# Kernel optimization log

Hardware: AMD Instinct MI355X
Metric: run time of the kernel (lower is better)

## Reference

```python
import jax, jax.numpy as jnp
import numpy as np
from jax import lax

NUM_VARS = 16384
NUM_CHECKS = 8192
BATCH = 32
MAX_ITER = 15
H_DENSITY = 0.001  # ~8 ones per column, LDPC-like Tanner graph


def setup_inputs() -> dict:
    key = jax.random.key(0)
    k_h, k_s, k_l = jax.random.split(key, 3)
    # Sparse binary parity-check matrix represented densely (same math).
    parity_matrix = (jax.random.uniform(k_h, (NUM_CHECKS, NUM_VARS)) < H_DENSITY).astype(jnp.float32)
    syndrome = jax.random.randint(k_s, (BATCH, NUM_CHECKS), 0, 2).astype(jnp.float32)
    channel_llrs = jax.random.normal(k_l, (BATCH, NUM_VARS), dtype=jnp.float32)
    w_vc = jnp.ones((1,), dtype=jnp.float32)
    w_cv = jnp.ones((1,), dtype=jnp.float32)
    damping = jnp.float32(0.5)
    return {
        "syndrome": syndrome,
        "parity_matrix": parity_matrix,
        "channel_llrs": channel_llrs,
        "w_vc": w_vc,
        "w_cv": w_cv,
        "damping": damping,
    }


def reference(syndrome, parity_matrix, channel_llrs, w_vc, w_cv, damping):
    # syndrome: (B, C); parity_matrix H: (C, V); channel_llrs: (B, V)
    s_sign = 1.0 - 2.0 * syndrome  # (B, C)

    def body(v_beliefs, _):
        # v -> c: sparse.mm(H, v^T)^T == v @ H^T  -> (B, C)
        v_to_c = w_vc * (v_beliefs @ parity_matrix.T)
        c_msg = s_sign * jnp.tanh(v_to_c * 0.5)  # (B, C)
        # c -> v: sparse.mm(H^T, c^T)^T == c @ H  -> (B, V)
        c_to_v = w_cv * (c_msg @ parity_matrix)
        v_new = damping * v_beliefs + (1.0 - damping) * (channel_llrs + c_to_v)
        return v_new, None

    v_beliefs, _ = lax.scan(body, channel_llrs, None, length=MAX_ITER)
    return jax.nn.sigmoid(-v_beliefs)  # (B, V) bit-flip probabilities
```

## Files before the change

### kernel.cpp

```cpp
#include <hip/hip_runtime.h>


#define C_NUM 8192
#define V_NUM 16384
#define B_NUM 32
#define ROW_SLOTS 40
#define COL_SLOTS 24

#define NBLK 256
#define NTHR 1024
#define NTH (NBLK * NTHR)

typedef unsigned short u16;
typedef unsigned int u32;
typedef unsigned long long u64;

__device__ __forceinline__ float agent_ldf(const float* p) {
    return __hip_atomic_load(p, __ATOMIC_RELAXED, __HIP_MEMORY_SCOPE_AGENT);
}
__device__ __forceinline__ void agent_stf(float* p, float v) {
    __hip_atomic_store(p, v, __ATOMIC_RELAXED, __HIP_MEMORY_SCOPE_AGENT);
}
__device__ __forceinline__ u32 agent_ld32(const u32* p) {
    return __hip_atomic_load(p, __ATOMIC_RELAXED, __HIP_MEMORY_SCOPE_AGENT);
}
__device__ __forceinline__ void agent_st32(u32* p, u32 v) {
    __hip_atomic_store(p, v, __ATOMIC_RELAXED, __HIP_MEMORY_SCOPE_AGENT);
}
__device__ __forceinline__ int agent_ldi(const int* p) {
    return __hip_atomic_load(p, __ATOMIC_RELAXED, __HIP_MEMORY_SCOPE_AGENT);
}
__device__ __forceinline__ void agent_st16(u16* p, u16 v) {
    __hip_atomic_store(p, v, __ATOMIC_RELAXED, __HIP_MEMORY_SCOPE_AGENT);
}

__device__ __forceinline__ void grid_barrier(u32* flags, u32 ep) {
    __syncthreads();
    if (threadIdx.x < 64) {
        if (threadIdx.x == 0) {
            asm volatile("s_waitcnt vmcnt(0) lgkmcnt(0)" ::: "memory");
            agent_st32(&flags[blockIdx.x], ep);
        }
        const int base = threadIdx.x * 4;
        for (;;) {
            u32 f0 = agent_ld32(&flags[base + 0]);
            u32 f1 = agent_ld32(&flags[base + 1]);
            u32 f2 = agent_ld32(&flags[base + 2]);
            u32 f3 = agent_ld32(&flags[base + 3]);
            bool ok = (f0 >= ep) & (f1 >= ep) & (f2 >= ep) & (f3 >= ep);
            if (__ballot(ok) == ~0ull) break;
            __builtin_amdgcn_s_sleep(2);
        }
        asm volatile("" ::: "memory");
    }
    __syncthreads();
}

__device__ __forceinline__ float fast_tanh_half(float x) {
    float ax = fabsf(x);
    float e = __expf(-ax);
    return copysignf((1.0f - e) / (1.0f + e), x);
}

__global__ __launch_bounds__(NTHR, 4)
void bp_fused(const float* __restrict__ H,
              const float* __restrict__ synd,
              const float* __restrict__ llr,
              const float* __restrict__ w_vc_p,
              const float* __restrict__ w_cv_p,
              const float* __restrict__ damp_p,
              int* __restrict__ row_cnt, int* __restrict__ col_cnt,
              u16* __restrict__ row_tab, u16* __restrict__ col_tab,
              float* __restrict__ bel, float* __restrict__ cms,
              u32* __restrict__ flags,
              float* __restrict__ out) {
    const int tid = blockIdx.x * NTHR + threadIdx.x;
    u32 ep = 1;

    {
        u32* zp = (u32*)row_cnt;
        for (int t = tid; t < (C_NUM + V_NUM); t += NTH) agent_st32(&zp[t], 0u);
    }
    float llr_r[2], bel_r[2];
#pragma unroll
    for (int r = 0; r < 2; ++r) {
        int i = tid + r * NTH;
        int b = i & 31, v = i >> 5;
        float x = llr[b * V_NUM + v];
        llr_r[r] = x; bel_r[r] = x;
        agent_stf(&bel[i + 32], x);
    }
    float ss_r;
    {
        int b = tid & 31, c = tid >> 5;
        ss_r = 1.0f - 2.0f * synd[b * C_NUM + c];
    }
    grid_barrier(flags, ep++);

    {
        const int total4 = C_NUM * V_NUM / 4;
        const float4* Hv = (const float4*)H;
        for (int t = tid; t < total4; t += 2 * NTH) {
            float4 h0 = Hv[t];
            float4 h1 = Hv[t + NTH];
#pragma unroll
            for (int half = 0; half < 2; ++half) {
                float4 hv = half ? h1 : h0;
                int base = (half ? (t + NTH) : t) * 4;
                float vals[4] = {hv.x, hv.y, hv.z, hv.w};
#pragma unroll
                for (int k = 0; k < 4; ++k) {
                    if (vals[k] != 0.0f) {
                        int ee = base + k;
                        int c = ee >> 14;
                        int v = ee & (V_NUM - 1);
                        int rs = atomicAdd(&row_cnt[c], 1);
                        if (rs < ROW_SLOTS)
                            agent_st16(&row_tab[c * ROW_SLOTS + rs], (u16)(v + 1));
                        int cs = atomicAdd(&col_cnt[v], 1);
                        if (cs < COL_SLOTS)
                            agent_st16(&col_tab[v * COL_SLOTS + cs], (u16)(c + 1));
                    }
                }
            }
        }
    }
    grid_barrier(flags, ep++);

    if (tid < C_NUM) {
        int c = tid;
        int n = agent_ldi(&row_cnt[c]); n = n > ROW_SLOTS ? ROW_SLOTS : n;
        for (int k = n; k < ROW_SLOTS; ++k)
            agent_st16(&row_tab[c * ROW_SLOTS + k],
                       (u16)((((c * 97) + (k * 131)) & (V_NUM - 1)) + 1));
    } else if (tid < C_NUM + V_NUM) {
        int v = tid - C_NUM;
        int n = agent_ldi(&col_cnt[v]); n = n > COL_SLOTS ? COL_SLOTS : n;
        for (int k = n; k < COL_SLOTS; ++k)
            agent_st16(&col_tab[v * COL_SLOTS + k],
                       (u16)((((v * 89) + (k * 61)) & (C_NUM - 1)) + 1));
    }
    const float wvc = w_vc_p[0];
    const float wcv = w_cv_p[0];
    const float d   = damp_p[0];
    const int b  = tid & 31;
    const int c0 = tid >> 5;
    int n_row;
    {
        int n = agent_ldi(&row_cnt[c0]);
        n_row = n > ROW_SLOTS ? ROW_SLOTS : n;
    }
    int n_col[2];
#pragma unroll
    for (int r = 0; r < 2; ++r) {
        int n = agent_ldi(&col_cnt[(tid + r * NTH) >> 5]);
        n_col[r] = n > COL_SLOTS ? COL_SLOTS : n;
    }
    grid_barrier(flags, ep++);

    for (int it = 0; it < 15; ++it) {
        {
            const u64* rt = (const u64*)(row_tab + (size_t)c0 * ROW_SLOTS);
            float sum = 0.0f;
#pragma unroll
            for (int p = 0; p < ROW_SLOTS / 4; ++p) {
                u64 q = rt[p];
                float v0 = agent_ldf(&bel[(int)(q & 0xFFFFu) * 32 + b]);
                float v1 = agent_ldf(&bel[(int)((q >> 16) & 0xFFFFu) * 32 + b]);
                float v2 = agent_ldf(&bel[(int)((q >> 32) & 0xFFFFu) * 32 + b]);
                float v3 = agent_ldf(&bel[(int)(q >> 48) * 32 + b]);
                int j = p * 4;
                sum += (j     < n_row) ? v0 : 0.0f;
                sum += (j + 1 < n_row) ? v1 : 0.0f;
                sum += (j + 2 < n_row) ? v2 : 0.0f;
                sum += (j + 3 < n_row) ? v3 : 0.0f;
            }
            agent_stf(&cms[tid + 32], ss_r * fast_tanh_half(wvc * sum));
        }
        grid_barrier(flags, ep++);

        bool last = (it == 14);
#pragma unroll
        for (int r = 0; r < 2; ++r) {
            int i = tid + r * NTH;
            int v = i >> 5;
            const u64* ct = (const u64*)(col_tab + (size_t)v * COL_SLOTS);
            float sum = 0.0f;
#pragma unroll
            for (int p = 0; p < COL_SLOTS / 4; ++p) {
                u64 q = ct[p];
                float v0 = agent_ldf(&cms[(int)(q & 0xFFFFu) * 32 + b]);
                float v1 = agent_ldf(&cms[(int)((q >> 16) & 0xFFFFu) * 32 + b]);
                float v2 = agent_ldf(&cms[(int)((q >> 32) & 0xFFFFu) * 32 + b]);
                float v3 = agent_ldf(&cms[(int)(q >> 48) * 32 + b]);
                int j = p * 4;
                sum += (j     < n_col[r]) ? v0 : 0.0f;
                sum += (j + 1 < n_col[r]) ? v1 : 0.0f;
                sum += (j + 2 < n_col[r]) ? v2 : 0.0f;
                sum += (j + 3 < n_col[r]) ? v3 : 0.0f;
            }
            float nb = d * bel_r[r] + (1.0f - d) * (llr_r[r] + wcv * sum);
            bel_r[r] = nb;
            if (!last) agent_stf(&bel[i + 32], nb);
            else       out[b * V_NUM + v] = 1.0f / (1.0f + __expf(nb));
        }
        if (!last) grid_barrier(flags, ep++);
    }
}

extern "C" void kernel_launch(void* const* d_in, const int* in_sizes, int n_in,
                              void* d_out, int out_size, void* d_ws, size_t ws_size,
                              hipStream_t stream) {
    const float* synd = (const float*)d_in[0];
    const float* H    = (const float*)d_in[1];
    const float* llr  = (const float*)d_in[2];
    const float* w_vc = (const float*)d_in[3];
    const float* w_cv = (const float*)d_in[4];
    const float* damp = (const float*)d_in[5];
    float* out = (float*)d_out;

    char* ws = (char*)d_ws;
    size_t off = 0;
    int* row_cnt = (int*)(ws + off); off += (size_t)C_NUM * 4;
    int* col_cnt = (int*)(ws + off); off += (size_t)V_NUM * 4;
    u16* row_tab = (u16*)(ws + off); off += (size_t)C_NUM * ROW_SLOTS * 2;
    u16* col_tab = (u16*)(ws + off); off += (size_t)V_NUM * COL_SLOTS * 2;
    float* bel = (float*)(ws + off); off += (size_t)(V_NUM + 1) * 32 * 4;
    float* cms = (float*)(ws + off); off += (size_t)(C_NUM + 1) * 32 * 4;
    u32* flags = (u32*)(ws + off); off += (size_t)NBLK * 4;

    hipMemsetAsync(flags, 0, (size_t)NBLK * 4, stream);

    void* args[] = {
        (void*)&H, (void*)&synd, (void*)&llr,
        (void*)&w_vc, (void*)&w_cv, (void*)&damp,
        (void*)&row_cnt, (void*)&col_cnt, (void*)&row_tab, (void*)&col_tab,
        (void*)&bel, (void*)&cms, (void*)&flags, (void*)&out
    };
    hipLaunchCooperativeKernel((const void*)bp_fused,
                               dim3(NBLK), dim3(NTHR), args, 0, stream);
}
```

Measured before the change: 1.031 ms.

## Split batch into two half-chains with split-phase barriers to overlap iterations

Splits the 32-sample batch into two independent 16-sample chains, each with its own belief/check buffers and barrier flags. Grid barriers become split arrive/wait so one chain's phase runs while the other chain's barrier settles. Adjacency indices are kept in registers across iterations, padding is replaced by guarded loads, block size is halved, and the output is transposed through shared memory for coalesced stores. This adds register pressure and more barrier traffic, and depends on the hidden barrier latency outweighing the extra synchronization.

```diff
diff --git a/kernel.cpp b/kernel.cpp
--- a/kernel.cpp
+++ b/kernel.cpp
@@ -3,12 +3,11 @@
 
 #define C_NUM 8192
 #define V_NUM 16384
-#define B_NUM 32
 #define ROW_SLOTS 40
 #define COL_SLOTS 24
 
 #define NBLK 256
-#define NTHR 1024
+#define NTHR 512
 #define NTH (NBLK * NTHR)
 
 typedef unsigned short u16;
@@ -21,26 +20,31 @@
 __device__ __forceinline__ void agent_stf(float* p, float v) {
     __hip_atomic_store(p, v, __ATOMIC_RELAXED, __HIP_MEMORY_SCOPE_AGENT);
 }
+__device__ __forceinline__ u64 agent_ld64(const u64* p) {
+    return __hip_atomic_load(p, __ATOMIC_RELAXED, __HIP_MEMORY_SCOPE_AGENT);
+}
+__device__ __forceinline__ int agent_ldi(const int* p) {
+    return __hip_atomic_load(p, __ATOMIC_RELAXED, __HIP_MEMORY_SCOPE_AGENT);
+}
 __device__ __forceinline__ u32 agent_ld32(const u32* p) {
     return __hip_atomic_load(p, __ATOMIC_RELAXED, __HIP_MEMORY_SCOPE_AGENT);
 }
 __device__ __forceinline__ void agent_st32(u32* p, u32 v) {
     __hip_atomic_store(p, v, __ATOMIC_RELAXED, __HIP_MEMORY_SCOPE_AGENT);
 }
-__device__ __forceinline__ int agent_ldi(const int* p) {
-    return __hip_atomic_load(p, __ATOMIC_RELAXED, __HIP_MEMORY_SCOPE_AGENT);
-}
 __device__ __forceinline__ void agent_st16(u16* p, u16 v) {
     __hip_atomic_store(p, v, __ATOMIC_RELAXED, __HIP_MEMORY_SCOPE_AGENT);
 }
 
-__device__ __forceinline__ void grid_barrier(u32* flags, u32 ep) {
+__device__ __forceinline__ void bar_arrive(u32* flags, u32 ep) {
     __syncthreads();
+    if (threadIdx.x == 0) {
+        asm volatile("s_waitcnt vmcnt(0) lgkmcnt(0)" ::: "memory");
+        agent_st32(&flags[blockIdx.x], ep);
+    }
+}
+__device__ __forceinline__ void bar_wait(u32* flags, u32 ep) {
     if (threadIdx.x < 64) {
-        if (threadIdx.x == 0) {
-            asm volatile("s_waitcnt vmcnt(0) lgkmcnt(0)" ::: "memory");
-            agent_st32(&flags[blockIdx.x], ep);
-        }
         const int base = threadIdx.x * 4;
         for (;;) {
             u32 f0 = agent_ld32(&flags[base + 0]);
@@ -49,7 +53,7 @@
             u32 f3 = agent_ld32(&flags[base + 3]);
             bool ok = (f0 >= ep) & (f1 >= ep) & (f2 >= ep) & (f3 >= ep);
             if (__ballot(ok) == ~0ull) break;
-            __builtin_amdgcn_s_sleep(2);
+            __builtin_amdgcn_s_sleep(1);
         }
         asm volatile("" ::: "memory");
     }
@@ -62,7 +66,7 @@
     return copysignf((1.0f - e) / (1.0f + e), x);
 }
 
-__global__ __launch_bounds__(NTHR, 4)
+__global__ __launch_bounds__(NTHR, 2)
 void bp_fused(const float* __restrict__ H,
               const float* __restrict__ synd,
               const float* __restrict__ llr,
@@ -71,36 +75,23 @@
               const float* __restrict__ damp_p,
               int* __restrict__ row_cnt, int* __restrict__ col_cnt,
               u16* __restrict__ row_tab, u16* __restrict__ col_tab,
-              float* __restrict__ bel, float* __restrict__ cms,
-              u32* __restrict__ flags,
+              float* __restrict__ belA, float* __restrict__ belB,
+              float* __restrict__ cmsA, float* __restrict__ cmsB,
+              u32* __restrict__ flagsA, u32* __restrict__ flagsB,
               float* __restrict__ out) {
-    const int tid = blockIdx.x * NTHR + threadIdx.x;
-    u32 ep = 1;
+    const int gtid = blockIdx.x * NTHR + threadIdx.x;
+    __shared__ float tile[16][33];
 
     {
         u32* zp = (u32*)row_cnt;
-        for (int t = tid; t < (C_NUM + V_NUM); t += NTH) agent_st32(&zp[t], 0u);
-    }
-    float llr_r[2], bel_r[2];
-#pragma unroll
-    for (int r = 0; r < 2; ++r) {
-        int i = tid + r * NTH;
-        int b = i & 31, v = i >> 5;
-        float x = llr[b * V_NUM + v];
-        llr_r[r] = x; bel_r[r] = x;
-        agent_stf(&bel[i + 32], x);
-    }
-    float ss_r;
-    {
-        int b = tid & 31, c = tid >> 5;
-        ss_r = 1.0f - 2.0f * synd[b * C_NUM + c];
-    }
-    grid_barrier(flags, ep++);
+        for (int t = gtid; t < (C_NUM + V_NUM); t += NTH) agent_st32(&zp[t], 0u);
+    }
+    bar_arrive(flagsA, 1); bar_wait(flagsA, 1);
 
     {
         const int total4 = C_NUM * V_NUM / 4;
         const float4* Hv = (const float4*)H;
-        for (int t = tid; t < total4; t += 2 * NTH) {
+        for (int t = gtid; t < total4; t += 2 * NTH) {
             float4 h0 = Hv[t];
             float4 h1 = Hv[t + NTH];
 #pragma unroll
@@ -116,95 +107,121 @@
                         int v = ee & (V_NUM - 1);
                         int rs = atomicAdd(&row_cnt[c], 1);
                         if (rs < ROW_SLOTS)
-                            agent_st16(&row_tab[c * ROW_SLOTS + rs], (u16)(v + 1));
+                            agent_st16(&row_tab[c * ROW_SLOTS + rs], (u16)v);
                         int cs = atomicAdd(&col_cnt[v], 1);
                         if (cs < COL_SLOTS)
-                            agent_st16(&col_tab[v * COL_SLOTS + cs], (u16)(c + 1));
+                            agent_st16(&col_tab[v * COL_SLOTS + cs], (u16)c);
                     }
                 }
             }
         }
     }
-    grid_barrier(flags, ep++);
-
-    if (tid < C_NUM) {
-        int c = tid;
-        int n = agent_ldi(&row_cnt[c]); n = n > ROW_SLOTS ? ROW_SLOTS : n;
-        for (int k = n; k < ROW_SLOTS; ++k)
-            agent_st16(&row_tab[c * ROW_SLOTS + k],
-                       (u16)((((c * 97) + (k * 131)) & (V_NUM - 1)) + 1));
-    } else if (tid < C_NUM + V_NUM) {
-        int v = tid - C_NUM;
-        int n = agent_ldi(&col_cnt[v]); n = n > COL_SLOTS ? COL_SLOTS : n;
-        for (int k = n; k < COL_SLOTS; ++k)
-            agent_st16(&col_tab[v * COL_SLOTS + k],
-                       (u16)((((v * 89) + (k * 61)) & (C_NUM - 1)) + 1));
-    }
+    bar_arrive(flagsA, 2); bar_wait(flagsA, 2);
+
+    const int b16 = gtid & 15;
+    const int c0  = gtid >> 4;
+    u64 rq[ROW_SLOTS / 4];
+#pragma unroll
+    for (int p = 0; p < ROW_SLOTS / 4; ++p)
+        rq[p] = agent_ld64((const u64*)(row_tab + (size_t)c0 * ROW_SLOTS) + p);
+    int n_row;
+    { int n = agent_ldi(&row_cnt[c0]); n_row = n > ROW_SLOTS ? ROW_SLOTS : n; }
+
+    u64 cq[2][COL_SLOTS / 4];
+    int n_col[2], v_r[2];
+    float llr_a[2], llr_b[2], bel_a[2], bel_b[2];
+#pragma unroll
+    for (int r = 0; r < 2; ++r) {
+        int v = (gtid + r * NTH) >> 4;
+        v_r[r] = v;
+#pragma unroll
+        for (int p = 0; p < COL_SLOTS / 4; ++p)
+            cq[r][p] = agent_ld64((const u64*)(col_tab + (size_t)v * COL_SLOTS) + p);
+        int n = agent_ldi(&col_cnt[v]);
+        n_col[r] = n > COL_SLOTS ? COL_SLOTS : n;
+        float xa = llr[b16 * V_NUM + v];
+        float xb = llr[(b16 + 16) * V_NUM + v];
+        llr_a[r] = xa; bel_a[r] = xa;
+        llr_b[r] = xb; bel_b[r] = xb;
+        agent_stf(&belA[v * 16 + b16], xa);
+        agent_stf(&belB[v * 16 + b16], xb);
+    }
+    const float ss_a = 1.0f - 2.0f * synd[b16 * C_NUM + c0];
+    const float ss_b = 1.0f - 2.0f * synd[(b16 + 16) * C_NUM + c0];
     const float wvc = w_vc_p[0];
     const float wcv = w_cv_p[0];
     const float d   = damp_p[0];
-    const int b  = tid & 31;
-    const int c0 = tid >> 5;
-    int n_row;
-    {
-        int n = agent_ldi(&row_cnt[c0]);
-        n_row = n > ROW_SLOTS ? ROW_SLOTS : n;
-    }
-    int n_col[2];
-#pragma unroll
-    for (int r = 0; r < 2; ++r) {
-        int n = agent_ldi(&col_cnt[(tid + r * NTH) >> 5]);
-        n_col[r] = n > COL_SLOTS ? COL_SLOTS : n;
-    }
-    grid_barrier(flags, ep++);
-
-    for (int it = 0; it < 15; ++it) {
-        {
-            const u64* rt = (const u64*)(row_tab + (size_t)c0 * ROW_SLOTS);
-            float sum = 0.0f;
-#pragma unroll
-            for (int p = 0; p < ROW_SLOTS / 4; ++p) {
-                u64 q = rt[p];
-                float v0 = agent_ldf(&bel[(int)(q & 0xFFFFu) * 32 + b]);
-                float v1 = agent_ldf(&bel[(int)((q >> 16) & 0xFFFFu) * 32 + b]);
-                float v2 = agent_ldf(&bel[(int)((q >> 32) & 0xFFFFu) * 32 + b]);
-                float v3 = agent_ldf(&bel[(int)(q >> 48) * 32 + b]);
-                int j = p * 4;
-                sum += (j     < n_row) ? v0 : 0.0f;
-                sum += (j + 1 < n_row) ? v1 : 0.0f;
-                sum += (j + 2 < n_row) ? v2 : 0.0f;
-                sum += (j + 3 < n_row) ? v3 : 0.0f;
-            }
-            agent_stf(&cms[tid + 32], ss_r * fast_tanh_half(wvc * sum));
-        }
-        grid_barrier(flags, ep++);
-
-        bool last = (it == 14);
+    bar_arrive(flagsA, 3); bar_wait(flagsA, 3);
+
+#define VC_PHASE(BEL, CMS, SS)                                               \
+    {                                                                        \
+        float sum = 0.0f;                                                    \
+        _Pragma("unroll")                                                    \
+        for (int p = 0; p < ROW_SLOTS / 4; ++p) {                            \
+            u64 q = rq[p];                                                   \
+            int j = 4 * p;                                                   \
+            if (j     < n_row) sum += agent_ldf(&BEL[(int)(q & 0xFFFFu) * 16 + b16]); \
+            if (j + 1 < n_row) sum += agent_ldf(&BEL[(int)((q >> 16) & 0xFFFFu) * 16 + b16]); \
+            if (j + 2 < n_row) sum += agent_ldf(&BEL[(int)((q >> 32) & 0xFFFFu) * 16 + b16]); \
+            if (j + 3 < n_row) sum += agent_ldf(&BEL[(int)(q >> 48) * 16 + b16]); \
+        }                                                                    \
+        agent_stf(&CMS[c0 * 16 + b16], (SS) * fast_tanh_half(wvc * sum));    \
+    }
+
+#define CV_PHASE(CMS, BELREG, LLRREG, BEL, LASTIT)                           \
+    {                                                                        \
+        _Pragma("unroll")                                                    \
+        for (int r = 0; r < 2; ++r) {                                        \
+            float sum = 0.0f;                                                \
+            _Pragma("unroll")                                                \
+            for (int p = 0; p < COL_SLOTS / 4; ++p) {                        \
+                u64 q = cq[r][p];                                            \
+                int j = 4 * p;                                               \
+                if (j     < n_col[r]) sum += agent_ldf(&CMS[(int)(q & 0xFFFFu) * 16 + b16]); \
+                if (j + 1 < n_col[r]) sum += agent_ldf(&CMS[(int)((q >> 16) & 0xFFFFu) * 16 + b16]); \
+                if (j + 2 < n_col[r]) sum += agent_ldf(&CMS[(int)((q >> 32) & 0xFFFFu) * 16 + b16]); \
+                if (j + 3 < n_col[r]) sum += agent_ldf(&CMS[(int)(q >> 48) * 16 + b16]); \
+            }                                                                \
+            float nb = d * BELREG[r] + (1.0f - d) * (LLRREG[r] + wcv * sum); \
+            BELREG[r] = nb;                                                  \
+            if (!(LASTIT)) agent_stf(&BEL[v_r[r] * 16 + b16], nb);           \
+        }                                                                    \
+    }
+
+    VC_PHASE(belA, cmsA, ss_a);  bar_arrive(flagsA, 4);
+    VC_PHASE(belB, cmsB, ss_b);  bar_arrive(flagsB, 1);
+    for (int t = 0; t < 15; ++t) {
+        bool last = (t == 14);
+        bar_wait(flagsA, 4 + 2 * t);
+        CV_PHASE(cmsA, bel_a, llr_a, belA, last);
+        if (!last) bar_arrive(flagsA, 5 + 2 * t);
+        bar_wait(flagsB, 1 + 2 * t);
+        CV_PHASE(cmsB, bel_b, llr_b, belB, last);
+        if (!last) bar_arrive(flagsB, 2 + 2 * t);
+        if (!last) {
+            bar_wait(flagsA, 5 + 2 * t);
+            VC_PHASE(belA, cmsA, ss_a);
+            bar_arrive(flagsA, 6 + 2 * t);
+            bar_wait(flagsB, 2 + 2 * t);
+            VC_PHASE(belB, cmsB, ss_b);
+            bar_arrive(flagsB, 3 + 2 * t);
+        }
+    }
+
+#pragma unroll
+    for (int chain = 0; chain < 2; ++chain) {
 #pragma unroll
         for (int r = 0; r < 2; ++r) {
-            int i = tid + r * NTH;
-            int v = i >> 5;
-            const u64* ct = (const u64*)(col_tab + (size_t)v * COL_SLOTS);
-            float sum = 0.0f;
-#pragma unroll
-            for (int p = 0; p < COL_SLOTS / 4; ++p) {
-                u64 q = ct[p];
-                float v0 = agent_ldf(&cms[(int)(q & 0xFFFFu) * 32 + b]);
-                float v1 = agent_ldf(&cms[(int)((q >> 16) & 0xFFFFu) * 32 + b]);
-                float v2 = agent_ldf(&cms[(int)((q >> 32) & 0xFFFFu) * 32 + b]);
-                float v3 = agent_ldf(&cms[(int)(q >> 48) * 32 + b]);
-                int j = p * 4;
-                sum += (j     < n_col[r]) ? v0 : 0.0f;
-                sum += (j + 1 < n_col[r]) ? v1 : 0.0f;
-                sum += (j + 2 < n_col[r]) ? v2 : 0.0f;
-                sum += (j + 3 < n_col[r]) ? v3 : 0.0f;
-            }
-            float nb = d * bel_r[r] + (1.0f - d) * (llr_r[r] + wcv * sum);
-            bel_r[r] = nb;
-            if (!last) agent_stf(&bel[i + 32], nb);
-            else       out[b * V_NUM + v] = 1.0f / (1.0f + __expf(nb));
-        }
-        if (!last) grid_barrier(flags, ep++);
+            __syncthreads();
+            float val = chain ? bel_b[r] : bel_a[r];
+            tile[b16][threadIdx.x >> 4] = val;
+            __syncthreads();
+            int brow = (threadIdx.x >> 5) + chain * 16;
+            int col  = threadIdx.x & 31;
+            int vbase = blockIdx.x * 32 + r * 8192;
+            float x = tile[threadIdx.x >> 5][col];
+            out[brow * V_NUM + vbase + col] = 1.0f / (1.0f + __expf(x));
+        }
     }
 }
 
@@ -225,17 +242,21 @@
     int* col_cnt = (int*)(ws + off); off += (size_t)V_NUM * 4;
     u16* row_tab = (u16*)(ws + off); off += (size_t)C_NUM * ROW_SLOTS * 2;
     u16* col_tab = (u16*)(ws + off); off += (size_t)V_NUM * COL_SLOTS * 2;
-    float* bel = (float*)(ws + off); off += (size_t)(V_NUM + 1) * 32 * 4;
-    float* cms = (float*)(ws + off); off += (size_t)(C_NUM + 1) * 32 * 4;
-    u32* flags = (u32*)(ws + off); off += (size_t)NBLK * 4;
-
-    hipMemsetAsync(flags, 0, (size_t)NBLK * 4, stream);
+    float* belA = (float*)(ws + off); off += (size_t)V_NUM * 16 * 4;
+    float* belB = (float*)(ws + off); off += (size_t)V_NUM * 16 * 4;
+    float* cmsA = (float*)(ws + off); off += (size_t)C_NUM * 16 * 4;
+    float* cmsB = (float*)(ws + off); off += (size_t)C_NUM * 16 * 4;
+    u32* flagsA = (u32*)(ws + off); off += (size_t)NBLK * 4;
+    u32* flagsB = (u32*)(ws + off); off += (size_t)NBLK * 4;
+
+    hipMemsetAsync(flagsA, 0, (size_t)NBLK * 2 * 4, stream);
 
     void* args[] = {
         (void*)&H, (void*)&synd, (void*)&llr,
         (void*)&w_vc, (void*)&w_cv, (void*)&damp,
         (void*)&row_cnt, (void*)&col_cnt, (void*)&row_tab, (void*)&col_tab,
-        (void*)&bel, (void*)&cms, (void*)&flags, (void*)&out
+        (void*)&belA, (void*)&belB, (void*)&cmsA, (void*)&cmsB,
+        (void*)&flagsA, (void*)&flagsB, (void*)&out
     };
     hipLaunchCooperativeKernel((const void*)bp_fused,
                                dim3(NBLK), dim3(NTHR), args, 0, stream);
```

Measured after the change: 1.464 ms. 1.42x slower.
